# Kernel optimization log

Measured on AMD Instinct MI355X. Metric: run time of the kernel, lower is better.

## Reference

```python
import jax, jax.numpy as jnp
import numpy as np

B, C, P, L = 16, 64, 128, 16        # batch, channels, patches, patch_length
D = 256                              # d_model / inner_dim
NPF = 256                            # num_poly_feats
NRFF = 128                           # num_rff
RFF_SCALE = 1.0
POLY_DEGREES = (2, 3)                # degree used is poly_degrees[i] - 2 -> (0, 1)
FEAT_DIM = L + NRFF + NPF * len(POLY_DEGREES)  # 16 + 128 + 512 = 656


def setup_inputs() -> dict:
    key = jax.random.key(0)
    ks = jax.random.split(key, 8)
    x = jax.random.normal(ks[0], (B, C, P, L), jnp.float32)
    # nn.Linear weights are (out_features, in_features); stacked over the 2 degrees
    Wq = jax.random.normal(ks[1], (2, D, L), jnp.float32) * 0.1
    Wk = jax.random.normal(ks[2], (2, D, L), jnp.float32) * 0.1
    Wv = jax.random.normal(ks[3], (2, NPF, L), jnp.float32) * 0.1
    freq_w = RFF_SCALE * jax.random.normal(ks[4], (L, NRFF // 2), jnp.float32)
    freq_b = jax.random.normal(ks[5], (1, 1, 1, NRFF // 2), jnp.float32)
    proj_w = jax.random.normal(ks[6], (D, FEAT_DIM), jnp.float32) * 0.02
    proj_b = jax.random.normal(ks[7], (D,), jnp.float32) * 0.02
    return {"x": x, "Wq": Wq, "Wk": Wk, "Wv": Wv,
            "freq_w": freq_w, "freq_b": freq_b,
            "proj_w": proj_w, "proj_b": proj_b}


def reference(x, Wq, Wk, Wv, freq_w, freq_b, proj_w, proj_b):
    # x: (B, C, P, L) -> transpose(1,2): attention runs over the channel axis
    xt = jnp.transpose(x, (0, 2, 1, 3))  # (B, P, C, L)
    polys = []
    for i, deg in enumerate((0, 1)):     # poly_degrees[i] - 2
        xp = xt ** deg                   # deg 0 -> ones, deg 1 -> xt
        Q = jnp.einsum('bpcl,dl->bpcd', xp, Wq[i])   # (B,P,C,D)
        K = jnp.einsum('bpcl,dl->bpcd', xt, Wk[i])   # (B,P,C,D)
        V = jnp.einsum('bpcl,fl->bpcf', xt, Wv[i])   # (B,P,C,NPF)
        S = jnp.einsum('bpcd,bped->bpce', Q, K)      # (B,P,C,C) un-normalized scores
        pf = jnp.einsum('bpce,bpef->bpcf', S, V)     # (B,P,C,NPF)
        polys.append(jnp.transpose(pf, (0, 2, 1, 3)))  # back to (B,C,P,NPF)
    polyfeats = jnp.concatenate(polys, axis=-1)      # (B,C,P,2*NPF)

    wx = x @ freq_w + freq_b                          # (B,C,P,NRFF//2)
    rff = jnp.concatenate([jnp.sin(wx), jnp.cos(wx)], axis=-1)  # (B,C,P,NRFF)

    feats = jnp.concatenate([x, polyfeats, rff], axis=-1)  # (B,C,P,FEAT_DIM)
    return feats @ proj_w.T + proj_b                        # (B,C,P,D)
```

## Files before the change

kernel.cpp:

```cpp
#include <hip/hip_runtime.h>
#include <hip/hip_bf16.h>

#define WS_WK0   0
#define WS_A     16
#define WS_E0    272
#define WS_BT    4368

typedef float f32x4 __attribute__((ext_vector_type(4)));
typedef short s16x8 __attribute__((ext_vector_type(8)));
typedef short s16x4 __attribute__((ext_vector_type(4)));

static __device__ __forceinline__ short bf16b(float f) {
  __hip_bfloat16 h = __float2bfloat16(f);
  return __builtin_bit_cast(short, h);
}

__global__ __launch_bounds__(512)
void pre_kernel(const float* __restrict__ Wq, const float* __restrict__ Wk,
                const float* __restrict__ Wv, const float* __restrict__ pw,
                float* __restrict__ ws)
{
  __shared__ float q0s[256];
  const int t = threadIdx.x;
  const int blk = blockIdx.x;
  ushort* bt = (ushort*)(ws + WS_BT);
  if (blk == 0) {
    if (t < 256) {
      float s = 0.f;
      #pragma unroll
      for (int l = 0; l < 16; ++l) s += Wq[t*16 + l];
      q0s[t] = s;
    }
    __syncthreads();
    if (t < 16) {
      float s = 0.f;
      for (int d = 0; d < 256; ++d) s += q0s[d] * Wk[d*16 + t];
      ws[WS_WK0 + t] = s;
    }
    if (t < 256) {
      const int l1 = t >> 4, l2 = t & 15;
      float s = 0.f;
      for (int d = 0; d < 256; ++d)
        s += Wq[4096 + d*16 + l1] * Wk[4096 + d*16 + l2];
      ws[WS_A + t] = s;
    }
  } else if (blk <= 8) {
    const int d = (blk-1)*32 + (t >> 4);
    const int l = t & 15;
    float s = 0.f;
    for (int f = 0; f < 256; ++f) s += pw[d*656 + 16 + f] * Wv[f*16 + l];
    ws[WS_E0 + d*16 + l] = s;
    bt[d*160 + l] = (ushort)bf16b(pw[d*656 + l]);
  } else if (blk <= 16) {
    const int d = (blk-9)*32 + (t >> 4);
    const int l = t & 15;
    float s = 0.f;
    for (int f = 0; f < 256; ++f) s += pw[d*656 + 272 + f] * Wv[4096 + f*16 + l];
    bt[d*160 + 16 + l] = (ushort)bf16b(s);
  } else {
    #pragma unroll 4
    for (int k = 0; k < 64; ++k) {
      const int e = k*512 + t;
      const int d = e >> 7, j = e & 127;
      const float v = (j < 64) ? pw[d*656 + 528 + j] : pw[d*656 + 592 + (j-64)];
      bt[d*160 + 32 + j] = (ushort)bf16b(v);
    }
  }
}

__global__ __launch_bounds__(256, 2)
void main_kernel(const float* __restrict__ x, const float* __restrict__ fw,
                 const float* __restrict__ fb, const float* __restrict__ pw,
                 const float* __restrict__ pb, const float* __restrict__ ws,
                 float* __restrict__ out)
{
  __shared__ float XsT[16*68];
  __shared__ float fws[16*64];
  __shared__ float fbs[64];
  __shared__ float Gs[256];
  __shared__ float N1s[256];
  __shared__ float tls[16];
  __shared__ float c0s[256];
  __shared__ short Abf[20*64*8];

  const int t = threadIdx.x;
  const int b = blockIdx.x >> 7;
  const int p = blockIdx.x & 127;

  {
    const int c = t >> 2, l0 = (t & 3) * 4;
    const float4 v = *(const float4*)(x + (((b*64 + c)*128 + p) << 4) + l0);
    XsT[(l0+0)*68 + c] = v.x;
    XsT[(l0+1)*68 + c] = v.y;
    XsT[(l0+2)*68 + c] = v.z;
    XsT[(l0+3)*68 + c] = v.w;
    s16x4 xb;
    xb[0] = bf16b(v.x); xb[1] = bf16b(v.y); xb[2] = bf16b(v.z); xb[3] = bf16b(v.w);
    *(s16x4*)&Abf[(((l0>>3)*64 + c) << 3) + (l0 & 4)] = xb;
  }
  *(float4*)(fws + t*4) = *(const float4*)(fw + t*4);
  if (t < 16) *(float4*)(fbs + t*4) = *(const float4*)(fb + t*4);
  __syncthreads();

  {
    const int l1 = t >> 4, l2 = t & 15;
    float g = 0.f;
    #pragma unroll
    for (int c = 0; c < 64; ++c) g += XsT[l1*68 + c] * XsT[l2*68 + c];
    Gs[t] = g;
  }
  {
    const int c = t & 63, jb = t >> 6;
    float sv[16], cv[16];
    #pragma unroll
    for (int k = 0; k < 16; ++k) {
      const int j = jb*16 + k;
      float wx = fbs[j];
      #pragma unroll
      for (int l = 0; l < 16; ++l) wx += XsT[l*68 + c] * fws[l*64 + j];
      __sincosf(wx, &sv[k], &cv[k]);
    }
    s16x8 pk;
    #pragma unroll
    for (int e = 0; e < 8; ++e) pk[e] = bf16b(sv[e]);
    *(s16x8*)&Abf[(((4 + 2*jb)*64 + c) << 3)] = pk;
    #pragma unroll
    for (int e = 0; e < 8; ++e) pk[e] = bf16b(sv[8+e]);
    *(s16x8*)&Abf[(((5 + 2*jb)*64 + c) << 3)] = pk;
    #pragma unroll
    for (int e = 0; e < 8; ++e) pk[e] = bf16b(cv[e]);
    *(s16x8*)&Abf[(((12 + 2*jb)*64 + c) << 3)] = pk;
    #pragma unroll
    for (int e = 0; e < 8; ++e) pk[e] = bf16b(cv[8+e]);
    *(s16x8*)&Abf[(((13 + 2*jb)*64 + c) << 3)] = pk;
  }
  __syncthreads();

  {
    const int l1 = t >> 4, l2 = t & 15;
    float s = 0.f;
    #pragma unroll
    for (int k = 0; k < 16; ++k) s += ws[WS_A + l1*16 + k] * Gs[k*16 + l2];
    N1s[t] = s;
  }
  if (t < 16) {
    float s = 0.f;
    #pragma unroll
    for (int k = 0; k < 16; ++k) s += Gs[t*16 + k] * ws[WS_WK0 + k];
    tls[t] = s;
  }
  __syncthreads();

  {
    const int c = t >> 2, lp0 = (t & 3) * 4;
    float m0 = 0.f, m1 = 0.f, m2 = 0.f, m3 = 0.f;
    #pragma unroll
    for (int l = 0; l < 16; ++l) {
      const float xv = XsT[l*68 + c];
      m0 += xv * N1s[l*16 + lp0];
      m1 += xv * N1s[l*16 + lp0+1];
      m2 += xv * N1s[l*16 + lp0+2];
      m3 += xv * N1s[l*16 + lp0+3];
    }
    s16x4 mb;
    mb[0] = bf16b(m0); mb[1] = bf16b(m1); mb[2] = bf16b(m2); mb[3] = bf16b(m3);
    *(s16x4*)&Abf[(((2 + (lp0>>3))*64 + c) << 3) + (lp0 & 4)] = mb;
  }
  {
    const int d = t;
    float s = pb[d];
    #pragma unroll
    for (int l = 0; l < 16; ++l) s += tls[l] * ws[WS_E0 + d*16 + l];
    c0s[d] = s;
  }
  __syncthreads();

  const int lane = t & 63, w = t >> 6;
  const int n0 = w << 6;
  const int lr = lane & 15, lq = lane >> 4;
  f32x4 acc[4][4] = {};
  const ushort* BT = (const ushort*)(ws + WS_BT);
  #pragma unroll
  for (int ks = 0; ks < 5; ++ks) {
    s16x8 af[4], bf_[4];
    #pragma unroll
    for (int mi = 0; mi < 4; ++mi)
      af[mi] = *(const s16x8*)&Abf[(((ks*4 + lq)*64) + mi*16 + lr) << 3];
    #pragma unroll
    for (int nt = 0; nt < 4; ++nt)
      bf_[nt] = *(const s16x8*)&BT[(n0 + nt*16 + lr)*160 + ks*32 + lq*8];
    #pragma unroll
    for (int mi = 0; mi < 4; ++mi)
      #pragma unroll
      for (int nt = 0; nt < 4; ++nt)
        acc[mi][nt] = __builtin_amdgcn_mfma_f32_16x16x32_bf16(af[mi], bf_[nt], acc[mi][nt], 0, 0, 0);
  }

  #pragma unroll
  for (int nt = 0; nt < 4; ++nt) {
    const int d = n0 + nt*16 + lr;
    const float cc = c0s[d];
    #pragma unroll
    for (int mi = 0; mi < 4; ++mi) {
      #pragma unroll
      for (int r = 0; r < 4; ++r) {
        const int c = mi*16 + lq*4 + r;
        out[(((b*64 + c)*128 + p) << 8) + d] = acc[mi][nt][r] + cc;
      }
    }
  }
}

extern "C" void kernel_launch(void* const* d_in, const int* in_sizes, int n_in,
                              void* d_out, int out_size, void* d_ws, size_t ws_size,
                              hipStream_t stream) {
  const float* x  = (const float*)d_in[0];
  const float* Wq = (const float*)d_in[1];
  const float* Wk = (const float*)d_in[2];
  const float* Wv = (const float*)d_in[3];
  const float* fw = (const float*)d_in[4];
  const float* fb = (const float*)d_in[5];
  const float* pw = (const float*)d_in[6];
  const float* pb = (const float*)d_in[7];
  float* out = (float*)d_out;
  float* ws  = (float*)d_ws;

  pre_kernel<<<18, 512, 0, stream>>>(Wq, Wk, Wv, pw, ws);
  main_kernel<<<16*128, 256, 0, stream>>>(x, fw, fb, pw, pb, ws, out);
}
```

Before: 53.51 us.

## Vectorize loads, swap MFMA operands for float4 output stores, restage pre-kernel via LDS

Swaps the A and B operands of the MFMA so each lane's accumulator holds four consecutive d values. The output can then be written with float4 stores instead of scalar stores. Also vectorizes many LDS and global reads in the main kernel (Gram matrix, RFF projection, N1 and c0 computation), and restages Wq/Wk/Wv through LDS in the pre-kernel so the dot products get coalesced float4 reads. The goal is fewer memory transactions, especially on the large output write, at the cost of more registers and larger LDS use in the pre-kernel.

```diff
diff --git a/kernel.cpp b/kernel.cpp
--- a/kernel.cpp
+++ b/kernel.cpp
@@ -20,48 +20,94 @@
                 const float* __restrict__ Wv, const float* __restrict__ pw,
                 float* __restrict__ ws)
 {
-  __shared__ float q0s[256];
+  __shared__ float lds[8448];
   const int t = threadIdx.x;
   const int blk = blockIdx.x;
   ushort* bt = (ushort*)(ws + WS_BT);
+
   if (blk == 0) {
+    {
+      const int d = t >> 1;
+      const int lb = (t & 1) * 8;
+      #pragma unroll
+      for (int h = 0; h < 2; ++h) {
+        const float4 vq = *(const float4*)(Wq + 4096 + t*8 + h*4);
+        lds[(lb+h*4+0)*256 + d] = vq.x;
+        lds[(lb+h*4+1)*256 + d] = vq.y;
+        lds[(lb+h*4+2)*256 + d] = vq.z;
+        lds[(lb+h*4+3)*256 + d] = vq.w;
+        const float4 vk = *(const float4*)(Wk + 4096 + t*8 + h*4);
+        lds[4096 + (lb+h*4+0)*256 + d] = vk.x;
+        lds[4096 + (lb+h*4+1)*256 + d] = vk.y;
+        lds[4096 + (lb+h*4+2)*256 + d] = vk.z;
+        lds[4096 + (lb+h*4+3)*256 + d] = vk.w;
+      }
+    }
     if (t < 256) {
       float s = 0.f;
       #pragma unroll
-      for (int l = 0; l < 16; ++l) s += Wq[t*16 + l];
-      q0s[t] = s;
+      for (int q = 0; q < 4; ++q) {
+        const float4 v = *(const float4*)(Wq + t*16 + q*4);
+        s += v.x + v.y + v.z + v.w;
+      }
+      lds[8192 + t] = s;
     }
     __syncthreads();
+    if (t < 256) {
+      const int l1 = t >> 4, l2 = t & 15;
+      const float* r1 = lds + l1*256;
+      const float* r2 = lds + 4096 + l2*256;
+      float s = 0.f;
+      #pragma unroll 8
+      for (int dq = 0; dq < 64; ++dq) {
+        const float4 a = *(const float4*)(r1 + dq*4);
+        const float4 b = *(const float4*)(r2 + dq*4);
+        s += a.x*b.x + a.y*b.y + a.z*b.z + a.w*b.w;
+      }
+      ws[WS_A + t] = s;
+    }
     if (t < 16) {
       float s = 0.f;
-      for (int d = 0; d < 256; ++d) s += q0s[d] * Wk[d*16 + t];
+      for (int d = 0; d < 256; ++d) s += lds[8192 + d] * Wk[d*16 + t];
       ws[WS_WK0 + t] = s;
     }
-    if (t < 256) {
-      const int l1 = t >> 4, l2 = t & 15;
-      float s = 0.f;
-      for (int d = 0; d < 256; ++d)
-        s += Wq[4096 + d*16 + l1] * Wk[4096 + d*16 + l2];
-      ws[WS_A + t] = s;
-    }
-  } else if (blk <= 8) {
-    const int d = (blk-1)*32 + (t >> 4);
+  } else if (blk <= 16) {
+    const int deg = (blk <= 8) ? 0 : 1;
+    {
+      const int f = t >> 1;
+      const int lb = (t & 1) * 8;
+      #pragma unroll
+      for (int h = 0; h < 2; ++h) {
+        const float4 v = *(const float4*)(Wv + deg*4096 + t*8 + h*4);
+        lds[(lb+h*4+0)*256 + f] = v.x;
+        lds[(lb+h*4+1)*256 + f] = v.y;
+        lds[(lb+h*4+2)*256 + f] = v.z;
+        lds[(lb+h*4+3)*256 + f] = v.w;
+      }
+    }
+    __syncthreads();
+    const int d = ((blk-1) & 7)*32 + (t >> 4);
     const int l = t & 15;
+    const float* pr = pw + d*656 + (deg ? 272 : 16);
+    const float* wv = lds + l*256;
     float s = 0.f;
-    for (int f = 0; f < 256; ++f) s += pw[d*656 + 16 + f] * Wv[f*16 + l];
-    ws[WS_E0 + d*16 + l] = s;
-    bt[d*160 + l] = (ushort)bf16b(pw[d*656 + l]);
-  } else if (blk <= 16) {
-    const int d = (blk-9)*32 + (t >> 4);
-    const int l = t & 15;
-    float s = 0.f;
-    for (int f = 0; f < 256; ++f) s += pw[d*656 + 272 + f] * Wv[4096 + f*16 + l];
-    bt[d*160 + 16 + l] = (ushort)bf16b(s);
+    #pragma unroll 8
+    for (int fq = 0; fq < 64; ++fq) {
+      const float4 a = *(const float4*)(pr + fq*4);
+      const float4 b = *(const float4*)(wv + fq*4);
+      s += a.x*b.x + a.y*b.y + a.z*b.z + a.w*b.w;
+    }
+    if (deg == 0) {
+      ws[WS_E0 + d*16 + l] = s;
+      bt[d*160 + l] = (ushort)bf16b(pw[d*656 + l]);
+    } else {
+      bt[d*160 + 16 + l] = (ushort)bf16b(s);
+    }
   } else {
     #pragma unroll 4
     for (int k = 0; k < 64; ++k) {
-      const int e = k*512 + t;
-      const int d = e >> 7, j = e & 127;
+      const int d = k*4 + (t >> 7);
+      const int j = t & 127;
       const float v = (j < 64) ? pw[d*656 + 528 + j] : pw[d*656 + 592 + (j-64)];
       bt[d*160 + 32 + j] = (ushort)bf16b(v);
     }
@@ -104,49 +150,83 @@
 
   {
     const int l1 = t >> 4, l2 = t & 15;
+    const float* r1 = XsT + l1*68;
+    const float* r2 = XsT + l2*68;
     float g = 0.f;
     #pragma unroll
-    for (int c = 0; c < 64; ++c) g += XsT[l1*68 + c] * XsT[l2*68 + c];
+    for (int cq = 0; cq < 16; ++cq) {
+      const float4 a = *(const float4*)(r1 + cq*4);
+      const float4 bb = *(const float4*)(r2 + cq*4);
+      g += a.x*bb.x + a.y*bb.y + a.z*bb.z + a.w*bb.w;
+    }
     Gs[t] = g;
   }
   {
     const int c = t & 63, jb = t >> 6;
-    float sv[16], cv[16];
-    #pragma unroll
-    for (int k = 0; k < 16; ++k) {
-      const int j = jb*16 + k;
-      float wx = fbs[j];
-      #pragma unroll
-      for (int l = 0; l < 16; ++l) wx += XsT[l*68 + c] * fws[l*64 + j];
-      __sincosf(wx, &sv[k], &cv[k]);
-    }
-    s16x8 pk;
-    #pragma unroll
-    for (int e = 0; e < 8; ++e) pk[e] = bf16b(sv[e]);
-    *(s16x8*)&Abf[(((4 + 2*jb)*64 + c) << 3)] = pk;
-    #pragma unroll
-    for (int e = 0; e < 8; ++e) pk[e] = bf16b(sv[8+e]);
-    *(s16x8*)&Abf[(((5 + 2*jb)*64 + c) << 3)] = pk;
-    #pragma unroll
-    for (int e = 0; e < 8; ++e) pk[e] = bf16b(cv[e]);
-    *(s16x8*)&Abf[(((12 + 2*jb)*64 + c) << 3)] = pk;
-    #pragma unroll
-    for (int e = 0; e < 8; ++e) pk[e] = bf16b(cv[8+e]);
-    *(s16x8*)&Abf[(((13 + 2*jb)*64 + c) << 3)] = pk;
+    float wx[16];
+    {
+      const float4 b0 = *(const float4*)(fbs + jb*16);
+      const float4 b1 = *(const float4*)(fbs + jb*16 + 4);
+      const float4 b2 = *(const float4*)(fbs + jb*16 + 8);
+      const float4 b3 = *(const float4*)(fbs + jb*16 + 12);
+      wx[0]=b0.x; wx[1]=b0.y; wx[2]=b0.z; wx[3]=b0.w;
+      wx[4]=b1.x; wx[5]=b1.y; wx[6]=b1.z; wx[7]=b1.w;
+      wx[8]=b2.x; wx[9]=b2.y; wx[10]=b2.z; wx[11]=b2.w;
+      wx[12]=b3.x; wx[13]=b3.y; wx[14]=b3.z; wx[15]=b3.w;
+    }
+    #pragma unroll
+    for (int l = 0; l < 16; ++l) {
+      const float xv = XsT[l*68 + c];
+      const float4 f0 = *(const float4*)(fws + l*64 + jb*16);
+      const float4 f1 = *(const float4*)(fws + l*64 + jb*16 + 4);
+      const float4 f2 = *(const float4*)(fws + l*64 + jb*16 + 8);
+      const float4 f3 = *(const float4*)(fws + l*64 + jb*16 + 12);
+      wx[0] += xv*f0.x; wx[1] += xv*f0.y; wx[2] += xv*f0.z; wx[3] += xv*f0.w;
+      wx[4] += xv*f1.x; wx[5] += xv*f1.y; wx[6] += xv*f1.z; wx[7] += xv*f1.w;
+      wx[8] += xv*f2.x; wx[9] += xv*f2.y; wx[10] += xv*f2.z; wx[11] += xv*f2.w;
+      wx[12] += xv*f3.x; wx[13] += xv*f3.y; wx[14] += xv*f3.z; wx[15] += xv*f3.w;
+    }
+    s16x8 ps0, ps1, pc0, pc1;
+    #pragma unroll
+    for (int k = 0; k < 8; ++k) {
+      float sv, cv;
+      __sincosf(wx[k], &sv, &cv);
+      ps0[k] = bf16b(sv); pc0[k] = bf16b(cv);
+    }
+    #pragma unroll
+    for (int k = 0; k < 8; ++k) {
+      float sv, cv;
+      __sincosf(wx[8+k], &sv, &cv);
+      ps1[k] = bf16b(sv); pc1[k] = bf16b(cv);
+    }
+    *(s16x8*)&Abf[(((4 + 2*jb)*64 + c) << 3)] = ps0;
+    *(s16x8*)&Abf[(((5 + 2*jb)*64 + c) << 3)] = ps1;
+    *(s16x8*)&Abf[(((12 + 2*jb)*64 + c) << 3)] = pc0;
+    *(s16x8*)&Abf[(((13 + 2*jb)*64 + c) << 3)] = pc1;
   }
   __syncthreads();
 
   {
     const int l1 = t >> 4, l2 = t & 15;
+    float a[16];
+    #pragma unroll
+    for (int q = 0; q < 4; ++q)
+      *(float4*)(a + q*4) = *(const float4*)(ws + WS_A + l1*16 + q*4);
     float s = 0.f;
     #pragma unroll
-    for (int k = 0; k < 16; ++k) s += ws[WS_A + l1*16 + k] * Gs[k*16 + l2];
+    for (int k = 0; k < 16; ++k) s += a[k] * Gs[k*16 + l2];
     N1s[t] = s;
   }
   if (t < 16) {
+    float wk[16], gr[16];
+    #pragma unroll
+    for (int q = 0; q < 4; ++q) {
+      *(float4*)(wk + q*4) = *(const float4*)(ws + WS_WK0 + q*4);
+      *(float4*)(gr + q*4) = *(const float4*)(Gs + t*16 + q*4);
+    }
     float s = 0.f;
     #pragma unroll
-    for (int k = 0; k < 16; ++k) s += Gs[t*16 + k] * ws[WS_WK0 + k];
+    for (int k = 0; k < 16; ++k) s += gr[k] * wk[k];
     tls[t] = s;
   }
   __syncthreads();
@@ -157,10 +237,8 @@
     #pragma unroll
     for (int l = 0; l < 16; ++l) {
       const float xv = XsT[l*68 + c];
-      m0 += xv * N1s[l*16 + lp0];
-      m1 += xv * N1s[l*16 + lp0+1];
-      m2 += xv * N1s[l*16 + lp0+2];
-      m3 += xv * N1s[l*16 + lp0+3];
+      const float4 n = *(const float4*)(N1s + l*16 + lp0);
+      m0 += xv * n.x; m1 += xv * n.y; m2 += xv * n.z; m3 += xv * n.w;
     }
     s16x4 mb;
     mb[0] = bf16b(m0); mb[1] = bf16b(m1); mb[2] = bf16b(m2); mb[3] = bf16b(m3);
@@ -168,9 +246,15 @@
   }
   {
     const int d = t;
+    float e[16], tl[16];
+    #pragma unroll
+    for (int q = 0; q < 4; ++q) {
+      *(float4*)(e + q*4) = *(const float4*)(ws + WS_E0 + d*16 + q*4);
+      *(float4*)(tl + q*4) = *(const float4*)(tls + q*4);
+    }
     float s = pb[d];
     #pragma unroll
-    for (int l = 0; l < 16; ++l) s += tls[l] * ws[WS_E0 + d*16 + l];
+    for (int l = 0; l < 16; ++l) s += tl[l] * e[l];
     c0s[d] = s;
   }
   __syncthreads();
@@ -179,16 +263,16 @@
   const int n0 = w << 6;
   const int lr = lane & 15, lq = lane >> 4;
   f32x4 acc[4][4] = {};
-  const ushort* BT = (const ushort*)(ws + WS_BT);
+  const ushort* BTW = (const ushort*)(ws + WS_BT);
   #pragma unroll
   for (int ks = 0; ks < 5; ++ks) {
     s16x8 af[4], bf_[4];
     #pragma unroll
     for (int mi = 0; mi < 4; ++mi)
-      af[mi] = *(const s16x8*)&Abf[(((ks*4 + lq)*64) + mi*16 + lr) << 3];
+      af[mi] = *(const s16x8*)&BTW[(n0 + mi*16 + lr)*160 + ks*32 + lq*8];
     #pragma unroll
     for (int nt = 0; nt < 4; ++nt)
-      bf_[nt] = *(const s16x8*)&BT[(n0 + nt*16 + lr)*160 + ks*32 + lq*8];
+      bf_[nt] = *(const s16x8*)&Abf[(((ks*4 + lq)*64) + nt*16 + lr) << 3];
     #pragma unroll
     for (int mi = 0; mi < 4; ++mi)
       #pragma unroll
@@ -196,17 +280,22 @@
         acc[mi][nt] = __builtin_amdgcn_mfma_f32_16x16x32_bf16(af[mi], bf_[nt], acc[mi][nt], 0, 0, 0);
   }
 
+  float4 cv[4];
+  #pragma unroll
+  for (int mi = 0; mi < 4; ++mi)
+    cv[mi] = *(const float4*)(c0s + n0 + mi*16 + (lq << 2));
   #pragma unroll
   for (int nt = 0; nt < 4; ++nt) {
-    const int d = n0 + nt*16 + lr;
-    const float cc = c0s[d];
+    const int c = nt*16 + lr;
+    float* rp = out + (((b*64 + c)*128 + p) << 8) + n0 + (lq << 2);
     #pragma unroll
     for (int mi = 0; mi < 4; ++mi) {
-      #pragma unroll
-      for (int r = 0; r < 4; ++r) {
-        const int c = mi*16 + lq*4 + r;
-        out[(((b*64 + c)*128 + p) << 8) + d] = acc[mi][nt][r] + cc;
-      }
+      float4 o;
+      o.x = acc[mi][nt][0] + cv[mi].x;
+      o.y = acc[mi][nt][1] + cv[mi].y;
+      o.z = acc[mi][nt][2] + cv[mi].z;
+      o.w = acc[mi][nt][3] + cv[mi].w;
+      *(float4*)(rp + mi*16) = o;
     }
   }
 }
```

Result: slower. 58.42 us (+9.2%).
